# Kernel optimization log

Measured on AMD Instinct MI355X. Metric: run time of the kernel, lower is better.

Reference implementation:

```python
import jax, jax.numpy as jnp
import numpy as np

D_MODEL = 1024
NUM_HEADS = 16
HEAD_DIM = D_MODEL // NUM_HEADS
B, S = 2, 2048


def setup_inputs() -> dict:
    key = jax.random.key(0)
    ks = jax.random.split(key, 11)
    scale = 1.0 / np.sqrt(D_MODEL)
    inp = {
        "Q": jax.random.normal(ks[0], (B, S, D_MODEL), jnp.float32),
        "K": jax.random.normal(ks[1], (B, S, D_MODEL), jnp.float32),
        "V": jax.random.normal(ks[2], (B, S, D_MODEL), jnp.float32),
        # Linear weights stored as [in, out] (transposed nn.Linear layout)
        "Wq": jax.random.normal(ks[3], (D_MODEL, D_MODEL), jnp.float32) * scale,
        "bq": jax.random.normal(ks[4], (D_MODEL,), jnp.float32) * scale,
        "Wk": jax.random.normal(ks[5], (D_MODEL, D_MODEL), jnp.float32) * scale,
        "bk": jax.random.normal(ks[6], (D_MODEL,), jnp.float32) * scale,
        "Wv": jax.random.normal(ks[7], (D_MODEL, D_MODEL), jnp.float32) * scale,
        "bv": jax.random.normal(ks[8], (D_MODEL,), jnp.float32) * scale,
        "Wo": jax.random.normal(ks[9], (D_MODEL, D_MODEL), jnp.float32) * scale,
        "bo": jax.random.normal(ks[10], (D_MODEL,), jnp.float32) * scale,
    }
    return inp


def _split_heads(x):
    # [B, S, D] -> [B, H, S, Dh]
    b, s, _ = x.shape
    return x.reshape(b, s, NUM_HEADS, HEAD_DIM).transpose(0, 2, 1, 3)


def reference(Q, K, V, Wq, bq, Wk, bk, Wv, bv, Wo, bo):
    q = _split_heads(Q @ Wq + bq)   # [B,H,S,Dh]
    k = _split_heads(K @ Wk + bk)
    v = _split_heads(V @ Wv + bv)
    scores = jnp.einsum("bhqd,bhkd->bhqk", q, k) / jnp.sqrt(
        jnp.asarray(HEAD_DIM, q.dtype))
    attn = jax.nn.softmax(scores, axis=-1)
    out = jnp.einsum("bhqk,bhkd->bhqd", attn, v)  # [B,H,S,Dh]
    out = out.transpose(0, 2, 1, 3).reshape(Q.shape[0], -1, D_MODEL)
    return out @ Wo + bo
```

## Files before the change

### kernel.cpp

```cpp
#include <hip/hip_runtime.h>
#include <hip/hip_bf16.h>

typedef short bf16x4 __attribute__((ext_vector_type(4)));
typedef short bf16x8 __attribute__((ext_vector_type(8)));
typedef float fp32x4 __attribute__((ext_vector_type(4)));

#define MFMA16(a, b, c) __builtin_amdgcn_mfma_f32_16x16x32_bf16(a, b, c, 0, 0, 0)

static __device__ __forceinline__ short f2bf(float f) {
    unsigned int b = __float_as_uint(f);
    b += 0x7fffu + ((b >> 16) & 1u);
    return (short)(b >> 16);
}

static __device__ __forceinline__ unsigned int cvt_pk_bf16(float lo, float hi) {
    unsigned int r;
    asm("v_cvt_pk_bf16_f32 %0, %1, %2" : "=v"(r) : "v"(lo), "v"(hi));
    return r;
}

static __device__ __forceinline__ void gload_lds16(const void* g, void* l) {
    __builtin_amdgcn_global_load_lds(
        (const __attribute__((address_space(1))) unsigned int*)g,
        (__attribute__((address_space(3))) unsigned int*)l, 16, 0, 0);
}

typedef unsigned int uint2v __attribute__((ext_vector_type(2)));

__global__ __launch_bounds__(256) void prepass(
    const float* __restrict__ W0, const float* __restrict__ W1,
    const float* __restrict__ W2, const float* __restrict__ W3,
    short* __restrict__ wbt,
    const float* __restrict__ Q, const float* __restrict__ K,
    const float* __restrict__ V,
    short* __restrict__ xq, short* __restrict__ xk, short* __restrict__ xv)
{
    __shared__ short t[64][68];
    const int tid = threadIdx.x;
    const int b   = blockIdx.x;

    if (b < 1024) {
        const int z = b >> 8;
        const float* W = (z == 0) ? W0 : (z == 1) ? W1 : (z == 2) ? W2 : W3;
        short* dst = wbt + (size_t)z * 1024 * 1024;
        const int k0 = (b & 15) * 64, n0 = ((b >> 4) & 15) * 64;

#pragma unroll
        for (int p = 0; p < 4; ++p) {
            int c = p * 256 + tid;
            int kr = c >> 4, seg = c & 15;
            fp32x4 f = *(const fp32x4*)&W[(k0 + kr) * 1024 + n0 + seg * 4];
            uint2v u;
            u.x = cvt_pk_bf16(f[0], f[1]);
            u.y = cvt_pk_bf16(f[2], f[3]);
            *(uint2v*)&t[kr][seg * 4] = u;
        }
        __syncthreads();
#pragma unroll
        for (int p = 0; p < 2; ++p) {
            int c = p * 256 + tid;
            int nr = c >> 3, ks = c & 7;
            bf16x8 v;
#pragma unroll
            for (int i = 0; i < 8; ++i) v[i] = t[ks * 8 + i][nr];
            *(bf16x8*)&dst[(n0 + nr) * 1024 + k0 + ks * 8] = v;
        }
    } else {
        const int c = b - 1024;
        const int z = c >> 9;
        const int x = c & 511;
        const float* src = (z == 0) ? Q : (z == 1) ? K : V;
        short* dst = (z == 0) ? xq : (z == 1) ? xk : xv;
        const int idx = x * 256 + tid;
#pragma unroll
        for (int it = 0; it < 4; ++it) {
            size_t base = ((size_t)it * 131072 + idx) * 8;
            fp32x4 a = *(const fp32x4*)&src[base];
            fp32x4 bb = *(const fp32x4*)&src[base + 4];
            uint2v u0, u1;
            u0.x = cvt_pk_bf16(a[0], a[1]);
            u0.y = cvt_pk_bf16(a[2], a[3]);
            u1.x = cvt_pk_bf16(bb[0], bb[1]);
            u1.y = cvt_pk_bf16(bb[2], bb[3]);
            *(uint2v*)&dst[base] = u0;
            *(uint2v*)&dst[base + 4] = u1;
        }
    }
}

struct GemmArgs {
    const void* X[3];
    const short* W;
    const float* bias[3];
    void* out[3];
};

template <bool XFP32, bool HEADED, bool M64>
__global__ __launch_bounds__(256) void gemm128(GemmArgs ga)
{
    __shared__ __align__(16) short lds_a[128 * 40];
    __shared__ __align__(16) short lds_b[128 * 32];

    const int tid  = threadIdx.x;
    const int lane = tid & 63;
    const int wv   = tid >> 6;
    const int l15  = lane & 15;
    const int quad = lane >> 4;
    const int wm   = (wv >> 1) * (M64 ? 32 : 64);
    const int wn   = (wv & 1) * 64;
    const int sread = (quad ^ ((l15 >> 1) & 3)) * 8;
    const int MI   = M64 ? 2 : 4;

    const int nwg = gridDim.x * gridDim.y * gridDim.z;
    const int lid = blockIdx.x + gridDim.x * (blockIdx.y + gridDim.y * blockIdx.z);
    const int swz = (lid & 7) * (nwg >> 3) + (lid >> 3);
    const int z   = M64 ? 0 : (swz >> 8);
    const int rem = M64 ? swz : (swz & 255);
    const int m0  = (rem >> 3) * (M64 ? 64 : 128);
    const int n0  = (rem & 7) * 128;

    const void*  Xv   = ga.X[z];
    const short* W    = ga.W + (size_t)z * 1024 * 1024;
    const float* bias = ga.bias[z];
    void* outv        = ga.out[z];

    fp32x4 acc[4][4];
#pragma unroll
    for (int i = 0; i < 4; ++i)
#pragma unroll
        for (int j = 0; j < 4; ++j)
#pragma unroll
            for (int r = 0; r < 4; ++r) acc[i][j][r] = 0.f;

    for (int k0 = 0; k0 < 1024; k0 += 32) {
        __syncthreads();
        if (XFP32) {
            const float* X = (const float*)Xv;
#pragma unroll
            for (int p = 0; p < 4; ++p) {
                int c = p * 256 + tid;
                int row = c >> 3, ks = c & 7;
                fp32x4 f = *(const fp32x4*)&X[(m0 + row) * 1024 + k0 + ks * 4];
                uint2v u;
                u.x = cvt_pk_bf16(f[0], f[1]);
                u.y = cvt_pk_bf16(f[2], f[3]);
                *(uint2v*)&lds_a[row * 40 + ks * 4] = u;
            }
        } else {
            const short* X = (const short*)Xv;
#pragma unroll
            for (int p = 0; p < (M64 ? 1 : 2); ++p) {
                int c = p * 256 + tid;
                int row = c >> 2, s = c & 3;
                int sc = s ^ ((row >> 1) & 3);
                gload_lds16(&X[(m0 + row) * 1024 + k0 + sc * 8],
                            &lds_a[(p * 256 + wv * 64) * 8]);
            }
        }
#pragma unroll
        for (int p = 0; p < 2; ++p) {
            int c = p * 256 + tid;
            int row = c >> 2, s = c & 3;
            int sc = s ^ ((row >> 1) & 3);
            gload_lds16(&W[(n0 + row) * 1024 + k0 + sc * 8],
                        &lds_b[(p * 256 + wv * 64) * 8]);
        }
        __syncthreads();

        bf16x8 af[4], bf[4];
#pragma unroll
        for (int i = 0; i < MI; ++i)
            af[i] = XFP32
                ? *(bf16x8*)&lds_a[(wm + i * 16 + l15) * 40 + quad * 8]
                : *(bf16x8*)&lds_a[(wm + i * 16 + l15) * 32 + sread];
#pragma unroll
        for (int j = 0; j < 4; ++j)
            bf[j] = *(bf16x8*)&lds_b[(wn + j * 16 + l15) * 32 + sread];
#pragma unroll
        for (int i = 0; i < MI; ++i)
#pragma unroll
            for (int j = 0; j < 4; ++j)
                acc[i][j] = MFMA16(af[i], bf[j], acc[i][j]);
    }

#pragma unroll
    for (int i = 0; i < MI; ++i)
#pragma unroll
        for (int j = 0; j < 4; ++j)
#pragma unroll
            for (int r = 0; r < 4; ++r) {
                int row = m0 + wm + i * 16 + quad * 4 + r;
                int col = n0 + wn + j * 16 + l15;
                float v = acc[i][j][r] + bias[col];
                if (HEADED) {
                    int b = row >> 11, s = row & 2047;
                    int h = col >> 6,  dh = col & 63;
                    ((short*)outv)[(((b * 16) + h) * 2048 + s) * 64 + dh] = f2bf(v);
                } else {
                    ((float*)outv)[row * 1024 + col] = v;
                }
            }
}

__global__ __launch_bounds__(256) void attention128(
    const short* __restrict__ q, const short* __restrict__ k,
    const short* __restrict__ v, short* __restrict__ ctx)
{
    __shared__ __align__(16) short lds_k[64 * 64];
    __shared__ __align__(16) short lds_vt[64 * 74];

    const int tid  = threadIdx.x;
    const int lane = tid & 63;
    const int wv   = tid >> 6;
    const int l15  = lane & 15;
    const int quad = lane >> 4;
    const int bh   = blockIdx.y;
    const int q0   = blockIdx.x * 128 + wv * 32;

    const short* qb = q + (size_t)bh * 2048 * 64;
    const short* kb = k + (size_t)bh * 2048 * 64;
    const short* vb = v + (size_t)bh * 2048 * 64;

    bf16x8 qf[2][2];
#pragma unroll
    for (int qt = 0; qt < 2; ++qt)
#pragma unroll
        for (int h2 = 0; h2 < 2; ++h2)
            qf[qt][h2] = *(const bf16x8*)
                &qb[(q0 + qt * 16 + l15) * 64 + h2 * 32 + quad * 8];

    fp32x4 O[2][4];
    fp32x4 rs4[2];
#pragma unroll
    for (int qt = 0; qt < 2; ++qt) {
#pragma unroll
        for (int g = 0; g < 4; ++g)
#pragma unroll
            for (int r = 0; r < 4; ++r) O[qt][g][r] = 0.f;
#pragma unroll
        for (int r = 0; r < 4; ++r) rs4[qt][r] = 0.f;
    }

    const float SCL2E = 0.125f * 1.44269504088896340736f;

    const int k2   = tid >> 3;
    const int seg  = tid & 7;
    const int kk0  = k2 * 2;
    const int pos0 = (kk0 & 32) + (((kk0 & 15) >> 2) << 3)
                   + (((kk0 >> 4) & 1) << 2) + (kk0 & 3);

    const int ksrc  = ((lane & 7) ^ (lane >> 3)) * 8;
    const int krowl = lane >> 3;
    const int kswz  = l15 & 7;

    for (int key0 = 0; key0 < 2048; key0 += 64) {
        __syncthreads();
        bf16x8 v0 = *(const bf16x8*)&vb[(key0 + kk0) * 64 + seg * 8];
        bf16x8 v1 = *(const bf16x8*)&vb[(key0 + kk0 + 1) * 64 + seg * 8];
#pragma unroll
        for (int p = 0; p < 2; ++p) {
            int row = p * 32 + wv * 8 + krowl;
            gload_lds16(&kb[(key0 + row) * 64 + ksrc],
                        &lds_k[(p * 32 + wv * 8) * 64]);
        }
#pragma unroll
        for (int i = 0; i < 8; ++i) {
            unsigned int w = (unsigned int)(unsigned short)v0[i]
                           | ((unsigned int)(unsigned short)v1[i] << 16);
            *(unsigned int*)&lds_vt[(seg * 8 + i) * 74 + pos0] = w;
        }
        __syncthreads();

        bf16x8 kf[4][2];
#pragma unroll
        for (int kc = 0; kc < 4; ++kc)
#pragma unroll
            for (int h2 = 0; h2 < 2; ++h2)
                kf[kc][h2] = *(bf16x8*)
                    &lds_k[(kc * 16 + l15) * 64 + (((h2 * 4 + quad) ^ kswz) * 8)];

        union { bf16x8 v; unsigned int u[4]; } pfr[2][2];
        __builtin_amdgcn_s_setprio(1);
#pragma unroll
        for (int qt = 0; qt < 2; ++qt) {
#pragma unroll
            for (int kc = 0; kc < 4; ++kc) {
                fp32x4 s;
#pragma unroll
                for (int r = 0; r < 4; ++r) s[r] = 0.f;
                s = MFMA16(kf[kc][0], qf[qt][0], s);
                s = MFMA16(kf[kc][1], qf[qt][1], s);
                fp32x4 p;
#pragma unroll
                for (int r = 0; r < 4; ++r) {
                    p[r] = __builtin_amdgcn_exp2f(s[r] * SCL2E);
                    rs4[qt][r] += p[r];
                }
                pfr[qt][kc >> 1].u[(kc & 1) * 2 + 0] = cvt_pk_bf16(p[0], p[1]);
                pfr[qt][kc >> 1].u[(kc & 1) * 2 + 1] = cvt_pk_bf16(p[2], p[3]);
            }
        }
        __builtin_amdgcn_s_setprio(0);

        __builtin_amdgcn_s_setprio(1);
#pragma unroll
        for (int g = 0; g < 4; ++g)
#pragma unroll
            for (int ks = 0; ks < 2; ++ks) {
                bf16x8 vf = *(bf16x8*)
                    &lds_vt[(g * 16 + l15) * 74 + ks * 32 + quad * 8];
#pragma unroll
                for (int qt = 0; qt < 2; ++qt)
                    O[qt][g] = MFMA16(pfr[qt][ks].v, vf, O[qt][g]);
            }
        __builtin_amdgcn_s_setprio(0);
    }

    const int b = bh >> 4, h = bh & 15;
#pragma unroll
    for (int qt = 0; qt < 2; ++qt) {
        float t = (rs4[qt][0] + rs4[qt][1]) + (rs4[qt][2] + rs4[qt][3]);
        t += __shfl_xor(t, 16);
        t += __shfl_xor(t, 32);
#pragma unroll
        for (int r = 0; r < 4; ++r) {
            float tot = __shfl(t, quad * 4 + r);
            float inv = 1.f / tot;
            int qq  = q0 + qt * 16 + quad * 4 + r;
            int row = b * 2048 + qq;
#pragma unroll
            for (int g = 0; g < 4; ++g) {
                int col = h * 64 + g * 16 + l15;
                ctx[row * 1024 + col] = f2bf(O[qt][g][r] * inv);
            }
        }
    }
}

extern "C" void kernel_launch(void* const* d_in, const int* in_sizes, int n_in,
                              void* d_out, int out_size, void* d_ws, size_t ws_size,
                              hipStream_t stream) {
    const float* Q  = (const float*)d_in[0];
    const float* K  = (const float*)d_in[1];
    const float* V  = (const float*)d_in[2];
    const float* Wq = (const float*)d_in[3];
    const float* bq = (const float*)d_in[4];
    const float* Wk = (const float*)d_in[5];
    const float* bk = (const float*)d_in[6];
    const float* Wv = (const float*)d_in[7];
    const float* bv = (const float*)d_in[8];
    const float* Wo = (const float*)d_in[9];
    const float* bo = (const float*)d_in[10];

    const size_t NEL = 4096ull * 1024ull;
    short* wbt  = (short*)d_ws;
    short* vbuf = wbt + 4 * 1024 * 1024;
    short* cbuf = vbuf + NEL;
    short* xq   = cbuf + NEL;
    short* xk   = xq + NEL;
    short* xv   = cbuf;
    short* qbuf = (short*)d_out;
    short* kbuf = (short*)d_out + NEL;

    const bool big_ws = ws_size >= (40ull << 20);

    dim3 blk(256);

    GemmArgs g1;
    g1.W = wbt;
    g1.bias[0] = bq; g1.bias[1] = bk; g1.bias[2] = bv;
    g1.out[0] = qbuf; g1.out[1] = kbuf; g1.out[2] = vbuf;
    if (big_ws) {
        hipLaunchKernelGGL(prepass, dim3(2560), blk, 0, stream,
                           Wq, Wk, Wv, Wo, wbt, Q, K, V, xq, xk, xv);
        g1.X[0] = xq; g1.X[1] = xk; g1.X[2] = xv;
        hipLaunchKernelGGL((gemm128<false, true, false>), dim3(8, 32, 3), blk,
                           0, stream, g1);
    } else {
        hipLaunchKernelGGL(prepass, dim3(1024), blk, 0, stream,
                           Wq, Wk, Wv, Wo, wbt, Q, K, V, xq, xk, xv);
        g1.X[0] = Q;  g1.X[1] = K;  g1.X[2] = V;
        hipLaunchKernelGGL((gemm128<true, true, false>), dim3(8, 32, 3), blk,
                           0, stream, g1);
    }

    hipLaunchKernelGGL(attention128, dim3(16, 32), blk, 0, stream,
                       qbuf, kbuf, vbuf, cbuf);

    GemmArgs g2;
    g2.X[0] = cbuf; g2.X[1] = cbuf; g2.X[2] = cbuf;
    g2.W = wbt + 3ull * 1024 * 1024;
    g2.bias[0] = bo; g2.bias[1] = bo; g2.bias[2] = bo;
    g2.out[0] = d_out; g2.out[1] = d_out; g2.out[2] = d_out;
    hipLaunchKernelGGL((gemm128<false, false, true>), dim3(8, 64, 1), blk, 0,
                       stream, g2);
}
```

Measured before the change: 218.0 us.

## Double-buffer K/V LDS tiles and software-pipeline QK softmax with PV accumulation

Splits the attention loop into a two-stage software pipeline with double-buffered LDS for K and transposed V. The QK^T and exp step for tile n+1 is interleaved with the PV MFMA accumulation for tile n, so the scheduler can overlap exp/VALU work with matrix ops. Loads are still issued between barriers, so global-load latency is not hidden. The change doubles LDS use and keeps two sets of P fragments live, which raises register pressure and may reduce occupancy.

```diff
diff --git a/kernel.cpp b/kernel.cpp
--- a/kernel.cpp
+++ b/kernel.cpp
@@ -206,8 +206,8 @@
     const short* __restrict__ q, const short* __restrict__ k,
     const short* __restrict__ v, short* __restrict__ ctx)
 {
-    __shared__ __align__(16) short lds_k[64 * 64];
-    __shared__ __align__(16) short lds_vt[64 * 74];
+    __shared__ __align__(16) short lds_k[2][64 * 64];
+    __shared__ __align__(16) short lds_vt[2][64 * 74];
 
     const int tid  = threadIdx.x;
     const int lane = tid & 63;
@@ -253,68 +253,104 @@
     const int krowl = lane >> 3;
     const int kswz  = l15 & 7;
 
-    for (int key0 = 0; key0 < 2048; key0 += 64) {
-        __syncthreads();
-        bf16x8 v0 = *(const bf16x8*)&vb[(key0 + kk0) * 64 + seg * 8];
-        bf16x8 v1 = *(const bf16x8*)&vb[(key0 + kk0 + 1) * 64 + seg * 8];
-#pragma unroll
-        for (int p = 0; p < 2; ++p) {
-            int row = p * 32 + wv * 8 + krowl;
-            gload_lds16(&kb[(key0 + row) * 64 + ksrc],
-                        &lds_k[(p * 32 + wv * 8) * 64]);
-        }
-#pragma unroll
-        for (int i = 0; i < 8; ++i) {
-            unsigned int w = (unsigned int)(unsigned short)v0[i]
-                           | ((unsigned int)(unsigned short)v1[i] << 16);
-            *(unsigned int*)&lds_vt[(seg * 8 + i) * 74 + pos0] = w;
-        }
-        __syncthreads();
-
-        bf16x8 kf[4][2];
-#pragma unroll
-        for (int kc = 0; kc < 4; ++kc)
-#pragma unroll
-            for (int h2 = 0; h2 < 2; ++h2)
-                kf[kc][h2] = *(bf16x8*)
-                    &lds_k[(kc * 16 + l15) * 64 + (((h2 * 4 + quad) ^ kswz) * 8)];
-
-        union { bf16x8 v; unsigned int u[4]; } pfr[2][2];
+    union P4 { bf16x8 v; unsigned int u[4]; };
+    P4 pA[2][2], pB[2][2];
+
+#define STAGE(key0, B) do {                                                   \
+    bf16x8 sv0 = *(const bf16x8*)&vb[((key0) + kk0) * 64 + seg * 8];          \
+    bf16x8 sv1 = *(const bf16x8*)&vb[((key0) + kk0 + 1) * 64 + seg * 8];      \
+    _Pragma("unroll")                                                         \
+    for (int p_ = 0; p_ < 2; ++p_) {                                          \
+        int row_ = p_ * 32 + wv * 8 + krowl;                                  \
+        gload_lds16(&kb[((key0) + row_) * 64 + ksrc],                         \
+                    &lds_k[B][(p_ * 32 + wv * 8) * 64]);                      \
+    }                                                                         \
+    _Pragma("unroll")                                                         \
+    for (int i_ = 0; i_ < 8; ++i_) {                                          \
+        unsigned int w_ = (unsigned int)(unsigned short)sv0[i_]               \
+                        | ((unsigned int)(unsigned short)sv1[i_] << 16);      \
+        *(unsigned int*)&lds_vt[B][(seg * 8 + i_) * 74 + pos0] = w_;          \
+    }                                                                         \
+} while (0)
+
+#define QKSM(B, P) do {                                                       \
+    bf16x8 kf[4][2];                                                          \
+    _Pragma("unroll")                                                         \
+    for (int kc = 0; kc < 4; ++kc)                                            \
+        _Pragma("unroll")                                                     \
+        for (int h2 = 0; h2 < 2; ++h2)                                        \
+            kf[kc][h2] = *(bf16x8*)&lds_k[B][(kc * 16 + l15) * 64             \
+                         + (((h2 * 4 + quad) ^ kswz) * 8)];                   \
+    _Pragma("unroll")                                                         \
+    for (int qt = 0; qt < 2; ++qt) {                                          \
+        _Pragma("unroll")                                                     \
+        for (int kc = 0; kc < 4; ++kc) {                                      \
+            fp32x4 s;                                                         \
+            _Pragma("unroll")                                                 \
+            for (int r = 0; r < 4; ++r) s[r] = 0.f;                           \
+            s = MFMA16(kf[kc][0], qf[qt][0], s);                              \
+            s = MFMA16(kf[kc][1], qf[qt][1], s);                              \
+            fp32x4 pp;                                                        \
+            _Pragma("unroll")                                                 \
+            for (int r = 0; r < 4; ++r) {                                     \
+                pp[r] = __builtin_amdgcn_exp2f(s[r] * SCL2E);                 \
+                rs4[qt][r] += pp[r];                                          \
+            }                                                                 \
+            P[qt][kc >> 1].u[(kc & 1) * 2 + 0] = cvt_pk_bf16(pp[0], pp[1]);   \
+            P[qt][kc >> 1].u[(kc & 1) * 2 + 1] = cvt_pk_bf16(pp[2], pp[3]);   \
+        }                                                                     \
+    }                                                                         \
+} while (0)
+
+#define PVACC(B, P) do {                                                      \
+    _Pragma("unroll")                                                         \
+    for (int g = 0; g < 4; ++g)                                               \
+        _Pragma("unroll")                                                     \
+        for (int ks = 0; ks < 2; ++ks) {                                      \
+            bf16x8 vf = *(bf16x8*)&lds_vt[B][(g * 16 + l15) * 74              \
+                        + ks * 32 + quad * 8];                                \
+            _Pragma("unroll")                                                 \
+            for (int qt = 0; qt < 2; ++qt)                                    \
+                O[qt][g] = MFMA16(P[qt][ks].v, vf, O[qt][g]);                 \
+        }                                                                     \
+} while (0)
+
+    STAGE(0, 0);
+    __syncthreads();
+    __builtin_amdgcn_s_setprio(1);
+    QKSM(0, pA);
+    __builtin_amdgcn_s_setprio(0);
+
+#pragma unroll 1
+    for (int tp = 0; tp < 15; ++tp) {
+        const int o = (tp * 2 + 1) * 64;
+        __syncthreads();
+        STAGE(o, 1);
+        __syncthreads();
         __builtin_amdgcn_s_setprio(1);
-#pragma unroll
-        for (int qt = 0; qt < 2; ++qt) {
-#pragma unroll
-            for (int kc = 0; kc < 4; ++kc) {
-                fp32x4 s;
-#pragma unroll
-                for (int r = 0; r < 4; ++r) s[r] = 0.f;
-                s = MFMA16(kf[kc][0], qf[qt][0], s);
-                s = MFMA16(kf[kc][1], qf[qt][1], s);
-                fp32x4 p;
-#pragma unroll
-                for (int r = 0; r < 4; ++r) {
-                    p[r] = __builtin_amdgcn_exp2f(s[r] * SCL2E);
-                    rs4[qt][r] += p[r];
-                }
-                pfr[qt][kc >> 1].u[(kc & 1) * 2 + 0] = cvt_pk_bf16(p[0], p[1]);
-                pfr[qt][kc >> 1].u[(kc & 1) * 2 + 1] = cvt_pk_bf16(p[2], p[3]);
-            }
-        }
+        QKSM(1, pB);
+        PVACC(0, pA);
         __builtin_amdgcn_s_setprio(0);
-
+        __syncthreads();
+        STAGE(o + 64, 0);
+        __syncthreads();
         __builtin_amdgcn_s_setprio(1);
-#pragma unroll
-        for (int g = 0; g < 4; ++g)
-#pragma unroll
-            for (int ks = 0; ks < 2; ++ks) {
-                bf16x8 vf = *(bf16x8*)
-                    &lds_vt[(g * 16 + l15) * 74 + ks * 32 + quad * 8];
-#pragma unroll
-                for (int qt = 0; qt < 2; ++qt)
-                    O[qt][g] = MFMA16(pfr[qt][ks].v, vf, O[qt][g]);
-            }
+        QKSM(0, pA);
+        PVACC(1, pB);
         __builtin_amdgcn_s_setprio(0);
     }
+    __syncthreads();
+    STAGE(31 * 64, 1);
+    __syncthreads();
+    __builtin_amdgcn_s_setprio(1);
+    QKSM(1, pB);
+    PVACC(0, pA);
+    PVACC(1, pB);
+    __builtin_amdgcn_s_setprio(0);
+
+#undef STAGE
+#undef QKSM
+#undef PVACC
 
     const int b = bh >> 4, h = bh & 15;
 #pragma unroll
```

New measurement: 228.3 us. 4.7% more time.
